# Kernel tuning notes

Measured on AMD Instinct MI355X. Metric: run time of the kernel, lower is better.

Reference implementation:

```python
import jax, jax.numpy as jnp
import numpy as np

N_COMPONENTS = 16
N_FEATURES = 64
N_SAMPLES = 200000


def setup_inputs() -> dict:
    key = jax.random.key(0)
    k_data, k_means, k_cov = jax.random.split(key, 3)
    data = jax.random.normal(k_data, (N_SAMPLES, N_FEATURES), dtype=jnp.float32)
    weights = jnp.ones((N_COMPONENTS,), dtype=jnp.float32) / N_COMPONENTS
    means = jax.random.normal(k_means, (N_COMPONENTS, N_FEATURES), dtype=jnp.float32)
    # SPD covariances: A A^T / d + I (module inits to identity; use realistic SPD here)
    A = jax.random.normal(k_cov, (N_COMPONENTS, N_FEATURES, N_FEATURES), dtype=jnp.float32)
    covariances = jnp.einsum('kij,klj->kil', A, A) / N_FEATURES + jnp.eye(N_FEATURES, dtype=jnp.float32)
    return {"data": data, "weights": weights, "means": means, "covariances": covariances}


def reference(data, weights, means, covariances):
    # data: [N, d]; weights: [K]; means: [K, d]; covariances: [K, d, d]
    d = data.shape[1]
    L = jnp.linalg.cholesky(covariances)                      # [K, d, d]
    diff = data[None, :, :] - means[:, None, :]               # [K, N, d]
    # Solve L y = diff^T per component (batched triangular solve)
    y = jax.scipy.linalg.solve_triangular(L, jnp.swapaxes(diff, -1, -2), lower=True)  # [K, d, N]
    maha = jnp.sum(y * y, axis=1)                             # [K, N]
    half_logdet = jnp.sum(jnp.log(jnp.diagonal(L, axis1=-2, axis2=-1)), axis=-1)      # [K]
    log2pi = jnp.log(jnp.array(2.0 * np.pi, dtype=data.dtype))
    log_probs = -0.5 * (maha + d * log2pi) - half_logdet[:, None]                     # [K, N]
    weighted_log_probs = log_probs + jnp.log(weights)[:, None]
    log_sum_exp = jax.scipy.special.logsumexp(weighted_log_probs, axis=0)             # [N]
    return jnp.sum(log_sum_exp)
```

## Files before the change

### kernel.cpp

```cpp
#include <hip/hip_runtime.h>
#include <hip/hip_bf16.h>
#include <math.h>

#define NF 64
#define NC 16
#define MAIN_BLOCKS 256
#define MAIN_WAVES  13
#define TPW 4

typedef __bf16 bf16x8 __attribute__((ext_vector_type(8)));
typedef float f32x4 __attribute__((ext_vector_type(4)));
typedef unsigned int u32;

__device__ __forceinline__ void stage16(const void* gsrc, void* ldst) {
    __builtin_amdgcn_global_load_lds(
        (const __attribute__((address_space(1))) u32*)gsrc,
        (__attribute__((address_space(3))) u32*)ldst,
        16, 0, 0);
}

__global__ __launch_bounds__(256) void gmm_precompute(
    const float* __restrict__ cov,
    const float* __restrict__ means,
    const float* __restrict__ weights,
    __hip_bfloat16* __restrict__ g,
    float* __restrict__ t,
    float* __restrict__ Cc)
{
    const int w = threadIdx.x >> 6;
    const int c = threadIdx.x & 63;
    const int k = blockIdx.x;

    __shared__ __align__(16) float LT[NF][68];
    __shared__ float Xs[NF][65];
    __shared__ __align__(16) float wb2[2][68];
    __shared__ __align__(16) float gw2[2][68];

    float a_loc[16];
    {
        const float* src = cov + (long)k * NF * NF + (w * 16) * NF + c;
        #pragma unroll
        for (int r = 0; r < 16; ++r)
            a_loc[r] = src[r * NF];
    }

    float rsq_loc[16];
    float logdiag = 0.0f;

    #pragma unroll 1
    for (int q = 0; q < 4; ++q) {
        #pragma unroll
        for (int jj = 0; jj < 16; ++jj) {
            float* wb = wb2[jj & 1];
            if (w == q) wb[c] = a_loc[jj];
            __syncthreads();
            const int j = q * 16 + jj;
            float ajc = wb[c];
            float d   = wb[j];
            float sq  = sqrtf(d);
            float rsq = __builtin_amdgcn_rcpf(sq);
            float rd  = __builtin_amdgcn_rcpf(d);
            logdiag += 0.5f * __logf(d);
            if (w == q) rsq_loc[jj] = rsq;
            LT[j][c] = ajc * rsq;
            float beta = ajc * rd;
            const float4* wv = (const float4*)(wb + w * 16);
            #pragma unroll
            for (int rr = 0; rr < 16; rr += 4) {
                float4 v = wv[rr >> 2];
                a_loc[rr]     = fmaf(-v.x, beta, a_loc[rr]);
                a_loc[rr + 1] = fmaf(-v.y, beta, a_loc[rr + 1]);
                a_loc[rr + 2] = fmaf(-v.z, beta, a_loc[rr + 2]);
                a_loc[rr + 3] = fmaf(-v.w, beta, a_loc[rr + 3]);
            }
        }
    }

    float s_loc[16];
    #pragma unroll
    for (int r = 0; r < 16; ++r)
        s_loc[r] = (w * 16 + r == c) ? 1.0f : 0.0f;

    #pragma unroll 1
    for (int q = 0; q < 4; ++q) {
        #pragma unroll
        for (int ii = 0; ii < 16; ++ii) {
            const int i = q * 16 + ii;
            float* gw = gw2[ii & 1];
            if (w == q) {
                float gv = s_loc[ii] * rsq_loc[ii];
                gw[c] = gv;
                Xs[i][c] = gv;
            }
            __syncthreads();
            float gc = gw[c];
            const float4* lv4 = (const float4*)(&LT[i][w * 16]);
            #pragma unroll
            for (int rr = 0; rr < 16; rr += 4) {
                float4 v = lv4[rr >> 2];
                s_loc[rr]     = fmaf(-v.x, gc, s_loc[rr]);
                s_loc[rr + 1] = fmaf(-v.y, gc, s_loc[rr + 1]);
                s_loc[rr + 2] = fmaf(-v.z, gc, s_loc[rr + 2]);
                s_loc[rr + 3] = fmaf(-v.w, gc, s_loc[rr + 3]);
            }
        }
    }
    __syncthreads();

    {
        __hip_bfloat16* grow = g + ((long)(k * NF + c)) * NF;
        #pragma unroll
        for (int h = 0; h < 2; ++h) {
            int jb = w * 2 + h;
            bf16x8 v;
            #pragma unroll
            for (int u = 0; u < 8; ++u)
                v[u] = (__bf16)Xs[c][jb * 8 + u];
            *(bf16x8*)(grow + ((jb ^ (c & 7)) * 8)) = v;
        }
    }

    if (w == 0) {
        const float* mu = means + k * NF;
        float a0 = 0.0f, a1 = 0.0f;
        #pragma unroll
        for (int j = 0; j < NF; j += 2) {
            a0 = fmaf(Xs[c][j],     mu[j],     a0);
            a1 = fmaf(Xs[c][j + 1], mu[j + 1], a1);
        }
        t[k * NF + c] = a0 + a1;
        if (c == 0)
            Cc[k] = __logf(weights[k]) - 0.5f * (float)NF * 1.8378770664093453f - logdiag;
    }
}

__global__ __launch_bounds__(832, 4) void gmm_main(
    const float* __restrict__ data,
    const char* __restrict__ gsw,
    const float* __restrict__ t,
    const float* __restrict__ Cc,
    float* __restrict__ partials,
    int nTiles, int N, int totalWaves)
{
    __shared__ __align__(16) char gbuf[NC * 8192];
    __shared__ __align__(16) float nt_lds[NC * NF];
    __shared__ float cc_lds[NC];

    const int tidx = threadIdx.x;
    const int w    = tidx >> 6;
    const int lane = tidx & 63;
    const int l15  = lane & 15;
    const int lg   = lane >> 4;

    for (int i = w; i < NC; i += MAIN_WAVES) {
        const char* src = gsw + (size_t)i * 8192;
        char* dst = gbuf + (size_t)i * 8192;
        #pragma unroll
        for (int u = 0; u < 8; ++u)
            stage16(src + u * 1024 + lane * 16, dst + u * 1024);
    }

    for (int i = tidx; i < NC * NF; i += 832) nt_lds[i] = -t[i];
    if (tidx < NC) cc_lds[tidx] = Cc[tidx];

    const int gid = blockIdx.x * MAIN_WAVES + w;

    int offA[4], offB[4];
    #pragma unroll
    for (int rc = 0; rc < 4; ++rc) {
        int row = rc * 16 + l15;
        offA[rc] = row * 128 + ((lg       ^ (l15 & 7)) * 16);
        offB[rc] = row * 128 + (((lg + 4) ^ (l15 & 7)) * 16);
    }

    bf16x8 xf[TPW][2];
    if (gid < nTiles) {
        const long base = (long)gid * (TPW * 16);
        #pragma unroll
        for (int st = 0; st < TPW; ++st) {
            long row = base + st * 16 + l15;
            if (row > (long)N - 1) row = (long)N - 1;
            const float* xp = data + row * NF + lg * 8;
            float4 a0 = *(const float4*)(xp);
            float4 a1 = *(const float4*)(xp + 4);
            float4 b0 = *(const float4*)(xp + 32);
            float4 b1 = *(const float4*)(xp + 36);
            bf16x8 f0, f1;
            f0[0] = (__bf16)a0.x; f0[1] = (__bf16)a0.y;
            f0[2] = (__bf16)a0.z; f0[3] = (__bf16)a0.w;
            f0[4] = (__bf16)a1.x; f0[5] = (__bf16)a1.y;
            f0[6] = (__bf16)a1.z; f0[7] = (__bf16)a1.w;
            f1[0] = (__bf16)b0.x; f1[1] = (__bf16)b0.y;
            f1[2] = (__bf16)b0.z; f1[3] = (__bf16)b0.w;
            f1[4] = (__bf16)b1.x; f1[5] = (__bf16)b1.y;
            f1[6] = (__bf16)b1.z; f1[7] = (__bf16)b1.w;
            xf[st][0] = f0;
            xf[st][1] = f1;
        }
    }

    __syncthreads();

    float wavePartial = 0.0f;

    #pragma unroll 1
    for (int tile = gid; tile < nTiles; tile += totalWaves) {
        const long base = (long)tile * (TPW * 16);
        if (tile != gid) {
            #pragma unroll
            for (int st = 0; st < TPW; ++st) {
                long row = base + st * 16 + l15;
                if (row > (long)N - 1) row = (long)N - 1;
                const float* xp = data + row * NF + lg * 8;
                float4 a0 = *(const float4*)(xp);
                float4 a1 = *(const float4*)(xp + 4);
                float4 b0 = *(const float4*)(xp + 32);
                float4 b1 = *(const float4*)(xp + 36);
                bf16x8 f0, f1;
                f0[0] = (__bf16)a0.x; f0[1] = (__bf16)a0.y;
                f0[2] = (__bf16)a0.z; f0[3] = (__bf16)a0.w;
                f0[4] = (__bf16)a1.x; f0[5] = (__bf16)a1.y;
                f0[6] = (__bf16)a1.z; f0[7] = (__bf16)a1.w;
                f1[0] = (__bf16)b0.x; f1[1] = (__bf16)b0.y;
                f1[2] = (__bf16)b0.z; f1[3] = (__bf16)b0.w;
                f1[4] = (__bf16)b1.x; f1[5] = (__bf16)b1.y;
                f1[6] = (__bf16)b1.z; f1[7] = (__bf16)b1.w;
                xf[st][0] = f0;
                xf[st][1] = f1;
            }
        }

        float m[TPW], s[TPW];
        #pragma unroll
        for (int st = 0; st < TPW; ++st) { m[st] = -INFINITY; s[st] = 0.0f; }

        #pragma unroll 2
        for (int kk = 0; kk < NC; ++kk) {
            float mah[TPW];
            #pragma unroll
            for (int st = 0; st < TPW; ++st) mah[st] = 0.0f;

            #pragma unroll
            for (int rc = 0; rc < 4; ++rc) {
                bf16x8 ga = *(const bf16x8*)(gbuf + kk * 8192 + offA[rc]);
                bf16x8 gb = *(const bf16x8*)(gbuf + kk * 8192 + offB[rc]);
                f32x4 ntv = *(const f32x4*)(&nt_lds[kk * NF + rc * 16 + lg * 4]);
                #pragma unroll
                for (int st = 0; st < TPW; ++st) {
                    f32x4 acc = ntv;
                    acc = __builtin_amdgcn_mfma_f32_16x16x32_bf16(ga, xf[st][0], acc, 0, 0, 0);
                    acc = __builtin_amdgcn_mfma_f32_16x16x32_bf16(gb, xf[st][1], acc, 0, 0, 0);
                    mah[st] = fmaf(acc[0], acc[0], mah[st]);
                    mah[st] = fmaf(acc[1], acc[1], mah[st]);
                    mah[st] = fmaf(acc[2], acc[2], mah[st]);
                    mah[st] = fmaf(acc[3], acc[3], mah[st]);
                }
            }

            float Ck = cc_lds[kk];
            #pragma unroll
            for (int st = 0; st < TPW; ++st) {
                float v = mah[st];
                v += __shfl_xor(v, 16);
                v += __shfl_xor(v, 32);
                float wlp = fmaf(-0.5f, v, Ck);
                float mo = m[st];
                float mn = fmaxf(mo, wlp);
                s[st] = s[st] * __expf(mo - mn) + __expf(wlp - mn);
                m[st] = mn;
            }
        }

        if (lg == 0) {
            #pragma unroll
            for (int st = 0; st < TPW; ++st) {
                long sid = base + st * 16 + l15;
                if (sid < (long)N)
                    wavePartial += m[st] + __logf(s[st]);
            }
        }
    }

    #pragma unroll
    for (int off = 1; off < 64; off <<= 1)
        wavePartial += __shfl_xor(wavePartial, off);
    if (lane == 0)
        partials[gid] = wavePartial;
}

__global__ __launch_bounds__(256) void gmm_reduce(
    const float* __restrict__ partials, int n, float* __restrict__ out)
{
    float s = 0.0f;
    for (int i = threadIdx.x; i < n; i += 256)
        s += partials[i];
    #pragma unroll
    for (int off = 1; off < 64; off <<= 1)
        s += __shfl_xor(s, off);
    __shared__ float sm[4];
    const int wave = threadIdx.x >> 6;
    const int lane = threadIdx.x & 63;
    if (lane == 0) sm[wave] = s;
    __syncthreads();
    if (threadIdx.x == 0)
        out[0] = (sm[0] + sm[1]) + (sm[2] + sm[3]);
}

extern "C" void kernel_launch(void* const* d_in, const int* in_sizes, int n_in,
                              void* d_out, int out_size, void* d_ws, size_t ws_size,
                              hipStream_t stream)
{
    const float* data    = (const float*)d_in[0];
    const float* weights = (const float*)d_in[1];
    const float* means   = (const float*)d_in[2];
    const float* cov     = (const float*)d_in[3];

    const int N = in_sizes[0] / NF;

    char* ws = (char*)d_ws;
    __hip_bfloat16* g = (__hip_bfloat16*)ws;
    float* t          = (float*)(ws + 131072);
    float* Cc         = (float*)(ws + 131072 + 4096);
    float* partials   = (float*)(ws + 131072 + 4096 + 64);

    const int nTiles     = (N + TPW * 16 - 1) / (TPW * 16);
    const int totalWaves = MAIN_BLOCKS * MAIN_WAVES;

    gmm_precompute<<<NC, 256, 0, stream>>>(cov, means, weights, g, t, Cc);
    gmm_main<<<MAIN_BLOCKS, 64 * MAIN_WAVES, 0, stream>>>(
        data, (const char*)g, t, Cc, partials, nTiles, N, totalWaves);
    gmm_reduce<<<1, 256, 0, stream>>>(partials, totalWaves, (float*)d_out);
}
```

Baseline: 69.10 us.

## Switch Mahalanobis GEMM to 32x32x16 MFMA with bias folded in as extra MFMA

Result: slower. 77.79 us (+12.6%).

```diff
diff --git a/kernel.cpp b/kernel.cpp
--- a/kernel.cpp
+++ b/kernel.cpp
@@ -6,10 +6,10 @@
 #define NC 16
 #define MAIN_BLOCKS 256
 #define MAIN_WAVES  13
-#define TPW 4
 
 typedef __bf16 bf16x8 __attribute__((ext_vector_type(8)));
 typedef float f32x4 __attribute__((ext_vector_type(4)));
+typedef float f32x16 __attribute__((ext_vector_type(16)));
 typedef unsigned int u32;
 
 __device__ __forceinline__ void stage16(const void* gsrc, void* ldst) {
@@ -149,8 +149,8 @@
     const int tidx = threadIdx.x;
     const int w    = tidx >> 6;
     const int lane = tidx & 63;
-    const int l15  = lane & 15;
-    const int lg   = lane >> 4;
+    const int l31  = lane & 31;
+    const int hi   = lane >> 5;
 
     for (int i = w; i < NC; i += MAIN_WAVES) {
         const char* src = gsw + (size_t)i * 8192;
@@ -159,45 +159,47 @@
         for (int u = 0; u < 8; ++u)
             stage16(src + u * 1024 + lane * 16, dst + u * 1024);
     }
-
     for (int i = tidx; i < NC * NF; i += 832) nt_lds[i] = -t[i];
     if (tidx < NC) cc_lds[tidx] = Cc[tidx];
 
     const int gid = blockIdx.x * MAIN_WAVES + w;
 
-    int offA[4], offB[4];
-    #pragma unroll
-    for (int rc = 0; rc < 4; ++rc) {
-        int row = rc * 16 + l15;
-        offA[rc] = row * 128 + ((lg       ^ (l15 & 7)) * 16);
-        offB[rc] = row * 128 + (((lg + 4) ^ (l15 & 7)) * 16);
-    }
-
-    bf16x8 xf[TPW][2];
-    if (gid < nTiles) {
-        const long base = (long)gid * (TPW * 16);
-        #pragma unroll
-        for (int st = 0; st < TPW; ++st) {
-            long row = base + st * 16 + l15;
+    int offG[2][4];
+    #pragma unroll
+    for (int mt = 0; mt < 2; ++mt) {
+        int row = mt * 32 + l31;
+        #pragma unroll
+        for (int ks = 0; ks < 4; ++ks)
+            offG[mt][ks] = row * 128 + (((ks * 2 + hi) ^ (row & 7)) * 16);
+    }
+
+    bf16x8 b4;
+    #pragma unroll
+    for (int u = 0; u < 8; ++u) b4[u] = (__bf16)0.0f;
+    if (hi == 0) b4[0] = (__bf16)1.0f;
+
+    bf16x8 xf[2][4];
+    auto loadx = [&](long base) {
+        #pragma unroll
+        for (int ct = 0; ct < 2; ++ct) {
+            long row = base + ct * 32 + l31;
             if (row > (long)N - 1) row = (long)N - 1;
-            const float* xp = data + row * NF + lg * 8;
-            float4 a0 = *(const float4*)(xp);
-            float4 a1 = *(const float4*)(xp + 4);
-            float4 b0 = *(const float4*)(xp + 32);
-            float4 b1 = *(const float4*)(xp + 36);
-            bf16x8 f0, f1;
-            f0[0] = (__bf16)a0.x; f0[1] = (__bf16)a0.y;
-            f0[2] = (__bf16)a0.z; f0[3] = (__bf16)a0.w;
-            f0[4] = (__bf16)a1.x; f0[5] = (__bf16)a1.y;
-            f0[6] = (__bf16)a1.z; f0[7] = (__bf16)a1.w;
-            f1[0] = (__bf16)b0.x; f1[1] = (__bf16)b0.y;
-            f1[2] = (__bf16)b0.z; f1[3] = (__bf16)b0.w;
-            f1[4] = (__bf16)b1.x; f1[5] = (__bf16)b1.y;
-            f1[6] = (__bf16)b1.z; f1[7] = (__bf16)b1.w;
-            xf[st][0] = f0;
-            xf[st][1] = f1;
-        }
-    }
+            const float* xp = data + row * NF + hi * 8;
+            #pragma unroll
+            for (int ks = 0; ks < 4; ++ks) {
+                float4 p0 = *(const float4*)(xp + ks * 16);
+                float4 p1 = *(const float4*)(xp + ks * 16 + 4);
+                bf16x8 f;
+                f[0] = (__bf16)p0.x; f[1] = (__bf16)p0.y;
+                f[2] = (__bf16)p0.z; f[3] = (__bf16)p0.w;
+                f[4] = (__bf16)p1.x; f[5] = (__bf16)p1.y;
+                f[6] = (__bf16)p1.z; f[7] = (__bf16)p1.w;
+                xf[ct][ks] = f;
+            }
+        }
+    };
+
+    if (gid < nTiles) loadx((long)gid * 64);
 
     __syncthreads();
 
@@ -205,79 +207,74 @@
 
     #pragma unroll 1
     for (int tile = gid; tile < nTiles; tile += totalWaves) {
-        const long base = (long)tile * (TPW * 16);
-        if (tile != gid) {
-            #pragma unroll
-            for (int st = 0; st < TPW; ++st) {
-                long row = base + st * 16 + l15;
-                if (row > (long)N - 1) row = (long)N - 1;
-                const float* xp = data + row * NF + lg * 8;
-                float4 a0 = *(const float4*)(xp);
-                float4 a1 = *(const float4*)(xp + 4);
-                float4 b0 = *(const float4*)(xp + 32);
-                float4 b1 = *(const float4*)(xp + 36);
-                bf16x8 f0, f1;
-                f0[0] = (__bf16)a0.x; f0[1] = (__bf16)a0.y;
-                f0[2] = (__bf16)a0.z; f0[3] = (__bf16)a0.w;
-                f0[4] = (__bf16)a1.x; f0[5] = (__bf16)a1.y;
-                f0[6] = (__bf16)a1.z; f0[7] = (__bf16)a1.w;
-                f1[0] = (__bf16)b0.x; f1[1] = (__bf16)b0.y;
-                f1[2] = (__bf16)b0.z; f1[3] = (__bf16)b0.w;
-                f1[4] = (__bf16)b1.x; f1[5] = (__bf16)b1.y;
-                f1[6] = (__bf16)b1.z; f1[7] = (__bf16)b1.w;
-                xf[st][0] = f0;
-                xf[st][1] = f1;
-            }
-        }
-
-        float m[TPW], s[TPW];
-        #pragma unroll
-        for (int st = 0; st < TPW; ++st) { m[st] = -INFINITY; s[st] = 0.0f; }
+        const long base = (long)tile * 64;
+        if (tile != gid) loadx(base);
+
+        float m0 = -INFINITY, m1 = -INFINITY, s0 = 0.0f, s1 = 0.0f;
 
         #pragma unroll 2
         for (int kk = 0; kk < NC; ++kk) {
-            float mah[TPW];
-            #pragma unroll
-            for (int st = 0; st < TPW; ++st) mah[st] = 0.0f;
-
-            #pragma unroll
-            for (int rc = 0; rc < 4; ++rc) {
-                bf16x8 ga = *(const bf16x8*)(gbuf + kk * 8192 + offA[rc]);
-                bf16x8 gb = *(const bf16x8*)(gbuf + kk * 8192 + offB[rc]);
-                f32x4 ntv = *(const f32x4*)(&nt_lds[kk * NF + rc * 16 + lg * 4]);
+            float tv0 = nt_lds[kk * NF + l31];
+            float tv1 = nt_lds[kk * NF + 32 + l31];
+            bf16x8 a4m0, a4m1;
+            #pragma unroll
+            for (int u = 0; u < 8; ++u) { a4m0[u] = (__bf16)0.0f; a4m1[u] = (__bf16)0.0f; }
+            if (hi == 0) { a4m0[0] = (__bf16)tv0; a4m1[0] = (__bf16)tv1; }
+
+            float mah0 = 0.0f, mah1 = 0.0f;
+            const char* gk = gbuf + kk * 8192;
+            #pragma unroll
+            for (int mt = 0; mt < 2; ++mt) {
+                bf16x8 gA0 = *(const bf16x8*)(gk + offG[mt][0]);
+                bf16x8 gA1 = *(const bf16x8*)(gk + offG[mt][1]);
+                bf16x8 gA2 = *(const bf16x8*)(gk + offG[mt][2]);
+                bf16x8 gA3 = *(const bf16x8*)(gk + offG[mt][3]);
+                bf16x8 a4  = mt ? a4m1 : a4m0;
                 #pragma unroll
-                for (int st = 0; st < TPW; ++st) {
-                    f32x4 acc = ntv;
-                    acc = __builtin_amdgcn_mfma_f32_16x16x32_bf16(ga, xf[st][0], acc, 0, 0, 0);
-                    acc = __builtin_amdgcn_mfma_f32_16x16x32_bf16(gb, xf[st][1], acc, 0, 0, 0);
-                    mah[st] = fmaf(acc[0], acc[0], mah[st]);
-                    mah[st] = fmaf(acc[1], acc[1], mah[st]);
-                    mah[st] = fmaf(acc[2], acc[2], mah[st]);
-                    mah[st] = fmaf(acc[3], acc[3], mah[st]);
+                for (int ct = 0; ct < 2; ++ct) {
+                    f32x16 acc;
+                    #pragma unroll
+                    for (int u = 0; u < 16; ++u) acc[u] = 0.0f;
+                    acc = __builtin_amdgcn_mfma_f32_32x32x16_bf16(gA0, xf[ct][0], acc, 0, 0, 0);
+                    acc = __builtin_amdgcn_mfma_f32_32x32x16_bf16(gA1, xf[ct][1], acc, 0, 0, 0);
+                    acc = __builtin_amdgcn_mfma_f32_32x32x16_bf16(gA2, xf[ct][2], acc, 0, 0, 0);
+                    acc = __builtin_amdgcn_mfma_f32_32x32x16_bf16(gA3, xf[ct][3], acc, 0, 0, 0);
+                    acc = __builtin_amdgcn_mfma_f32_32x32x16_bf16(a4,  b4,        acc, 0, 0, 0);
+                    float q0 = 0.0f, q1 = 0.0f, q2 = 0.0f, q3 = 0.0f;
+                    #pragma unroll
+                    for (int u = 0; u < 16; u += 4) {
+                        q0 = fmaf(acc[u],     acc[u],     q0);
+                        q1 = fmaf(acc[u + 1], acc[u + 1], q1);
+                        q2 = fmaf(acc[u + 2], acc[u + 2], q2);
+                        q3 = fmaf(acc[u + 3], acc[u + 3], q3);
+                    }
+                    float qs = (q0 + q1) + (q2 + q3);
+                    if (ct == 0) mah0 += qs; else mah1 += qs;
                 }
             }
+            mah0 += __shfl_xor(mah0, 32);
+            mah1 += __shfl_xor(mah1, 32);
 
             float Ck = cc_lds[kk];
-            #pragma unroll
-            for (int st = 0; st < TPW; ++st) {
-                float v = mah[st];
-                v += __shfl_xor(v, 16);
-                v += __shfl_xor(v, 32);
-                float wlp = fmaf(-0.5f, v, Ck);
-                float mo = m[st];
-                float mn = fmaxf(mo, wlp);
-                s[st] = s[st] * __expf(mo - mn) + __expf(wlp - mn);
-                m[st] = mn;
-            }
-        }
-
-        if (lg == 0) {
-            #pragma unroll
-            for (int st = 0; st < TPW; ++st) {
-                long sid = base + st * 16 + l15;
-                if (sid < (long)N)
-                    wavePartial += m[st] + __logf(s[st]);
-            }
+            {
+                float wlp = fmaf(-0.5f, mah0, Ck);
+                float mn = fmaxf(m0, wlp);
+                s0 = s0 * __expf(m0 - mn) + __expf(wlp - mn);
+                m0 = mn;
+            }
+            {
+                float wlp = fmaf(-0.5f, mah1, Ck);
+                float mn = fmaxf(m1, wlp);
+                s1 = s1 * __expf(m1 - mn) + __expf(wlp - mn);
+                m1 = mn;
+            }
+        }
+
+        if (hi == 0) {
+            long sid0 = base + l31;
+            long sid1 = base + 32 + l31;
+            if (sid0 < (long)N) wavePartial += m0 + __logf(s0);
+            if (sid1 < (long)N) wavePartial += m1 + __logf(s1);
         }
     }
 
@@ -323,7 +320,7 @@
     float* Cc         = (float*)(ws + 131072 + 4096);
     float* partials   = (float*)(ws + 131072 + 4096 + 64);
 
-    const int nTiles     = (N + TPW * 16 - 1) / (TPW * 16);
+    const int nTiles     = (N + 63) / 64;
     const int totalWaves = MAIN_BLOCKS * MAIN_WAVES;
 
     gmm_precompute<<<NC, 256, 0, stream>>>(cov, means, weights, g, t, Cc);
```

## Skip zero upper-triangle MFMAs, rotate component order per wave, use 16 waves

Applied to the files above, without the earlier changes.

New measurement: 67.11 us. 2.9% less time.

```diff
diff --git a/kernel.cpp b/kernel.cpp
--- a/kernel.cpp
+++ b/kernel.cpp
@@ -5,7 +5,7 @@
 #define NF 64
 #define NC 16
 #define MAIN_BLOCKS 256
-#define MAIN_WAVES  13
+#define MAIN_WAVES  16
 #define TPW 4
 
 typedef __bf16 bf16x8 __attribute__((ext_vector_type(8)));
@@ -134,7 +134,7 @@
     }
 }
 
-__global__ __launch_bounds__(832, 4) void gmm_main(
+__global__ __launch_bounds__(1024) void gmm_main(
     const float* __restrict__ data,
     const char* __restrict__ gsw,
     const float* __restrict__ t,
@@ -152,15 +152,15 @@
     const int l15  = lane & 15;
     const int lg   = lane >> 4;
 
-    for (int i = w; i < NC; i += MAIN_WAVES) {
-        const char* src = gsw + (size_t)i * 8192;
-        char* dst = gbuf + (size_t)i * 8192;
+    {
+        const char* src = gsw + (size_t)w * 8192;
+        char* dst = gbuf + (size_t)w * 8192;
         #pragma unroll
         for (int u = 0; u < 8; ++u)
             stage16(src + u * 1024 + lane * 16, dst + u * 1024);
     }
 
-    for (int i = tidx; i < NC * NF; i += 832) nt_lds[i] = -t[i];
+    nt_lds[tidx] = -t[tidx];
     if (tidx < NC) cc_lds[tidx] = Cc[tidx];
 
     const int gid = blockIdx.x * MAIN_WAVES + w;
@@ -235,16 +235,34 @@
         for (int st = 0; st < TPW; ++st) { m[st] = -INFINITY; s[st] = 0.0f; }
 
         #pragma unroll 2
-        for (int kk = 0; kk < NC; ++kk) {
+        for (int ii = 0; ii < NC; ++ii) {
+            const int kk = (ii + w) & (NC - 1);
             float mah[TPW];
             #pragma unroll
             for (int st = 0; st < TPW; ++st) mah[st] = 0.0f;
 
-            #pragma unroll
-            for (int rc = 0; rc < 4; ++rc) {
-                bf16x8 ga = *(const bf16x8*)(gbuf + kk * 8192 + offA[rc]);
-                bf16x8 gb = *(const bf16x8*)(gbuf + kk * 8192 + offB[rc]);
-                f32x4 ntv = *(const f32x4*)(&nt_lds[kk * NF + rc * 16 + lg * 4]);
+            const char* gk = gbuf + kk * 8192;
+            const float* ntk = &nt_lds[kk * NF];
+
+            #pragma unroll
+            for (int rc = 0; rc < 2; ++rc) {
+                bf16x8 ga = *(const bf16x8*)(gk + offA[rc]);
+                f32x4 ntv = *(const f32x4*)(ntk + rc * 16 + lg * 4);
+                #pragma unroll
+                for (int st = 0; st < TPW; ++st) {
+                    f32x4 acc = ntv;
+                    acc = __builtin_amdgcn_mfma_f32_16x16x32_bf16(ga, xf[st][0], acc, 0, 0, 0);
+                    mah[st] = fmaf(acc[0], acc[0], mah[st]);
+                    mah[st] = fmaf(acc[1], acc[1], mah[st]);
+                    mah[st] = fmaf(acc[2], acc[2], mah[st]);
+                    mah[st] = fmaf(acc[3], acc[3], mah[st]);
+                }
+            }
+            #pragma unroll
+            for (int rc = 2; rc < 4; ++rc) {
+                bf16x8 ga = *(const bf16x8*)(gk + offA[rc]);
+                bf16x8 gb = *(const bf16x8*)(gk + offB[rc]);
+                f32x4 ntv = *(const f32x4*)(ntk + rc * 16 + lg * 4);
                 #pragma unroll
                 for (int st = 0; st < TPW; ++st) {
                     f32x4 acc = ntv;
```
